# Kernel tuning notes

Hardware: AMD Instinct MI355X
Metric: run time of the kernel (lower is better)

The kernel has to match this reference:

```python
import jax, jax.numpy as jnp
import numpy as np

N = 100000      # nodes
E = 1000000     # edges
IN = 128        # input features
H = 64          # hidden_channels
EPS = 1e-5      # BatchNorm eps


def _gcn_conv(x, W, b, src, dst, n):
    # PyG GCNConv: linear -> add self loops -> sym-norm -> scatter-add -> bias
    h = x @ W                                   # [n, H]
    loop = jnp.arange(n)
    s = jnp.concatenate([src, loop])            # [E+n]
    d = jnp.concatenate([dst, loop])
    deg = jax.ops.segment_sum(jnp.ones(s.shape, h.dtype), d, num_segments=n)
    dinv = jnp.where(deg > 0, jax.lax.rsqrt(deg), 0.0)
    norm = dinv[s] * dinv[d]                    # [E+n]
    out = jax.ops.segment_sum(h[s] * norm[:, None], d, num_segments=n)
    return out + b


def _bn_relu(x, gamma, beta):
    # BatchNorm1d, training-mode batch statistics (biased var), then ReLU
    m = x.mean(axis=0)
    v = x.var(axis=0)
    return jax.nn.relu((x - m) * jax.lax.rsqrt(v + EPS) * gamma + beta)


def setup_inputs() -> dict:
    key = jax.random.key(0)
    ks = jax.random.split(key, 10)
    x = jax.random.normal(ks[0], (N, IN), jnp.float32)
    edge_index = jax.random.randint(ks[1], (2, E), 0, N)
    W1 = jax.random.normal(ks[2], (IN, H), jnp.float32) / np.sqrt(IN)
    b1 = jnp.zeros((H,), jnp.float32)
    g1 = jnp.ones((H,), jnp.float32)
    bt1 = jnp.zeros((H,), jnp.float32)
    W2 = jax.random.normal(ks[3], (H, H), jnp.float32) / np.sqrt(H)
    b2 = jnp.zeros((H,), jnp.float32)
    g2 = jnp.ones((H,), jnp.float32)
    bt2 = jnp.zeros((H,), jnp.float32)
    return {"x": x, "edge_index": edge_index, "W1": W1, "b1": b1,
            "g1": g1, "bt1": bt1, "W2": W2, "b2": b2, "g2": g2, "bt2": bt2}


def reference(x, edge_index, W1, b1, g1, bt1, W2, b2, g2, bt2):
    src, dst = edge_index[0], edge_index[1]
    n = x.shape[0]
    h = _gcn_conv(x, W1, b1, src, dst, n)
    h = _bn_relu(h, g1, bt1)          # dropout omitted (deterministic reference)
    h = _gcn_conv(h, W2, b2, src, dst, n)
    h = _bn_relu(h, g2, bt2)
    return h
```

## Files before the change

kernel.cpp:

```cpp
#include <hip/hip_runtime.h>


#define IN_F 128
#define HID  64
#define SCAN_CHUNK 512
static constexpr float BN_EPS = 1e-5f;

typedef float f32x4 __attribute__((ext_vector_type(4)));
typedef short bf16x8 __attribute__((ext_vector_type(8)));

__device__ inline unsigned short f2bf(float f) {
    union { float f; unsigned u; } v; v.f = f;
    unsigned r = v.u + 0x7FFFu + ((v.u >> 16) & 1u);
    return (unsigned short)(r >> 16);
}
__device__ inline float bf2f(unsigned short h) {
    union { unsigned u; float f; } v; v.u = (unsigned)h << 16;
    return v.f;
}
__device__ inline float bflo(unsigned v) {
    union { unsigned u; float f; } x; x.u = v << 16; return x.f;
}
__device__ inline float bfhi(unsigned v) {
    union { unsigned u; float f; } x; x.u = v & 0xffff0000u; return x.f;
}


__global__ void count_dst(const int* __restrict__ dst, int* __restrict__ counts, int E) {
    int e = blockIdx.x * blockDim.x + threadIdx.x;
    if (e < E) atomicAdd(&counts[dst[e]], 1);
}

__global__ void scan_block_reduce(const int* __restrict__ counts, int* __restrict__ blockSums, int n) {
    __shared__ int red[256];
    int base = blockIdx.x * SCAN_CHUNK;
    int t = threadIdx.x;
    int i0 = base + 2 * t, i1 = i0 + 1;
    int v = 0;
    if (i0 < n) v += counts[i0];
    if (i1 < n) v += counts[i1];
    red[t] = v;
    __syncthreads();
    for (int st = 128; st > 0; st >>= 1) {
        if (t < st) red[t] += red[t + st];
        __syncthreads();
    }
    if (t == 0) blockSums[blockIdx.x] = red[0];
}

__global__ void scan_top(const int* __restrict__ blockSums, int* __restrict__ blockOffs, int B) {
    __shared__ int a[2][256];
    int t = threadIdx.x;
    int v = (t < B) ? blockSums[t] : 0;
    int pin = 0;
    a[0][t] = v;
    __syncthreads();
    for (int st = 1; st < 256; st <<= 1) {
        int x = a[pin][t];
        if (t >= st) x += a[pin][t - st];
        a[pin ^ 1][t] = x;
        pin ^= 1;
        __syncthreads();
    }
    if (t < B) blockOffs[t] = a[pin][t] - v;
}

__global__ void scan_write(const int* __restrict__ counts, const int* __restrict__ blockOffs,
                           int* __restrict__ ptr, int* __restrict__ cursor,
                           float* __restrict__ dinv, int n) {
    __shared__ int a[2][256];
    int base = blockIdx.x * SCAN_CHUNK;
    int t = threadIdx.x;
    int i0 = base + 2 * t, i1 = i0 + 1;
    int c0 = (i0 < n) ? counts[i0] : 0;
    int c1 = (i1 < n) ? counts[i1] : 0;
    int s = c0 + c1;
    int pin = 0;
    a[0][t] = s;
    __syncthreads();
    for (int st = 1; st < 256; st <<= 1) {
        int x = a[pin][t];
        if (t >= st) x += a[pin][t - st];
        a[pin ^ 1][t] = x;
        pin ^= 1;
        __syncthreads();
    }
    int excl = a[pin][t] - s + blockOffs[blockIdx.x];
    if (i0 < n) {
        ptr[i0] = excl; cursor[i0] = excl;
        dinv[i0] = rsqrtf((float)c0 + 1.0f);
    }
    if (i1 < n) {
        ptr[i1] = excl + c0; cursor[i1] = excl + c0;
        dinv[i1] = rsqrtf((float)c1 + 1.0f);
    }
}

__global__ void fill_csr(const int* __restrict__ src, const int* __restrict__ dst,
                         int* __restrict__ cursor, int* __restrict__ csr, int E) {
    int e = blockIdx.x * blockDim.x + threadIdx.x;
    if (e < E) {
        int pos = atomicAdd(&cursor[dst[e]], 1);
        csr[pos] = src[e];
    }
}


__global__ void convert_w(const float* __restrict__ W1, const float* __restrict__ W2,
                          unsigned short* __restrict__ W1t, unsigned short* __restrict__ W2t) {
    int t = threadIdx.x;
    for (int i = t; i < HID * IN_F; i += 256) {
        int c = i >> 7, k = i & 127;
        W1t[i] = f2bf(W1[k * HID + c]);
    }
    for (int i = t; i < HID * HID; i += 256) {
        int c = i >> 6, k = i & 63;
        W2t[i] = f2bf(W2[k * HID + c]);
    }
}


template <int K>
__global__ __launch_bounds__(256) void mfma_gemm_x(
    const float* __restrict__ X, const unsigned short* __restrict__ Wt,
    const float* __restrict__ dinv, unsigned short* __restrict__ out, int n) {
    constexpr int KS = K / 32;
    int t = threadIdx.x;
    int lane = t & 63, l15 = lane & 15, lhi = lane >> 4;
    bf16x8 Bf[4][KS];
#pragma unroll
    for (int cb = 0; cb < 4; ++cb)
#pragma unroll
        for (int ks = 0; ks < KS; ++ks)
            Bf[cb][ks] = *(const bf16x8*)&Wt[(cb * 16 + l15) * K + ks * 32 + lhi * 8];

    int wid = blockIdx.x * 4 + (t >> 6);
    int ntiles = n >> 4;
    if (wid >= ntiles) return;
    int r0 = wid << 4;
    const float* xrow = X + (size_t)(r0 + l15) * K;
    bf16x8 Af[KS];
#pragma unroll
    for (int ks = 0; ks < KS; ++ks) {
        float4 u = *(const float4*)&xrow[ks * 32 + lhi * 8];
        float4 v = *(const float4*)&xrow[ks * 32 + lhi * 8 + 4];
        bf16x8 a;
        a[0] = f2bf(u.x); a[1] = f2bf(u.y); a[2] = f2bf(u.z); a[3] = f2bf(u.w);
        a[4] = f2bf(v.x); a[5] = f2bf(v.y); a[6] = f2bf(v.z); a[7] = f2bf(v.w);
        Af[ks] = a;
    }
    f32x4 acc[4] = {{0.f,0.f,0.f,0.f},{0.f,0.f,0.f,0.f},{0.f,0.f,0.f,0.f},{0.f,0.f,0.f,0.f}};
#pragma unroll
    for (int cb = 0; cb < 4; ++cb)
#pragma unroll
        for (int ks = 0; ks < KS; ++ks)
            acc[cb] = __builtin_amdgcn_mfma_f32_16x16x32_bf16(Af[ks], Bf[cb][ks], acc[cb], 0, 0, 0);
#pragma unroll
    for (int j = 0; j < 4; ++j) {
        int r = r0 + lhi * 4 + j;
        float dv = dinv[r];
#pragma unroll
        for (int cb = 0; cb < 4; ++cb)
            out[(size_t)r * HID + cb * 16 + l15] = f2bf(acc[cb][j] * dv);
    }
}

__global__ __launch_bounds__(256) void mfma_gemm_bn(
    const float* __restrict__ V, const float* __restrict__ stats,
    const float* __restrict__ g, const float* __restrict__ beta,
    const unsigned short* __restrict__ Wt, const float* __restrict__ dinv,
    unsigned short* __restrict__ out, int n) {
    int t = threadIdx.x;
    int lane = t & 63, l15 = lane & 15, lhi = lane >> 4;
    bf16x8 Bf[4][2];
#pragma unroll
    for (int cb = 0; cb < 4; ++cb)
#pragma unroll
        for (int ks = 0; ks < 2; ++ks)
            Bf[cb][ks] = *(const bf16x8*)&Wt[(cb * 16 + l15) * HID + ks * 32 + lhi * 8];

    float aK[2][8], bK[2][8];
    float inv_n = 1.0f / (float)n;
#pragma unroll
    for (int ks = 0; ks < 2; ++ks)
#pragma unroll
        for (int e = 0; e < 8; ++e) {
            int k = ks * 32 + lhi * 8 + e;
            float m = stats[k] * inv_n;
            float var = stats[HID + k] * inv_n - m * m;
            float a = g[k] * rsqrtf(var + BN_EPS);
            aK[ks][e] = a;
            bK[ks][e] = beta[k] - m * a;
        }

    int wid = blockIdx.x * 4 + (t >> 6);
    int ntiles = n >> 4;
    if (wid >= ntiles) return;
    int r0 = wid << 4;
    const float* vrow = V + (size_t)(r0 + l15) * HID;
    bf16x8 Af[2];
#pragma unroll
    for (int ks = 0; ks < 2; ++ks) {
        float4 u = *(const float4*)&vrow[ks * 32 + lhi * 8];
        float4 v = *(const float4*)&vrow[ks * 32 + lhi * 8 + 4];
        float y[8] = {u.x, u.y, u.z, u.w, v.x, v.y, v.z, v.w};
        bf16x8 a;
#pragma unroll
        for (int e = 0; e < 8; ++e)
            a[e] = f2bf(fmaxf(fmaf(y[e], aK[ks][e], bK[ks][e]), 0.0f));
        Af[ks] = a;
    }
    f32x4 acc[4] = {{0.f,0.f,0.f,0.f},{0.f,0.f,0.f,0.f},{0.f,0.f,0.f,0.f},{0.f,0.f,0.f,0.f}};
#pragma unroll
    for (int cb = 0; cb < 4; ++cb)
#pragma unroll
        for (int ks = 0; ks < 2; ++ks)
            acc[cb] = __builtin_amdgcn_mfma_f32_16x16x32_bf16(Af[ks], Bf[cb][ks], acc[cb], 0, 0, 0);
#pragma unroll
    for (int j = 0; j < 4; ++j) {
        int r = r0 + lhi * 4 + j;
        float dv = dinv[r];
#pragma unroll
        for (int cb = 0; cb < 4; ++cb)
            out[(size_t)r * HID + cb * 16 + l15] = f2bf(acc[cb][j] * dv);
    }
}


__global__ __launch_bounds__(256) void aggregate_stats_bf(
    const unsigned short* __restrict__ hs, const float* __restrict__ dinv,
    const int* __restrict__ ptr, const int* __restrict__ counts,
    const int* __restrict__ csr, float* __restrict__ agg,
    float* __restrict__ stats, int n) {
    int t = threadIdx.x;
    int lane32 = t & 31;
    int grp = (blockIdx.x * blockDim.x + t) >> 5;
    int ngrp = (gridDim.x * blockDim.x) >> 5;
    float sx = 0.f, sy = 0.f, s2x = 0.f, s2y = 0.f;
    for (int i = grp; i < n; i += ngrp) {
        unsigned v = *(const unsigned*)&hs[(size_t)i * HID + 2 * lane32];
        float ax = bflo(v), ay = bfhi(v);
        float bx = 0.f, by = 0.f, cx = 0.f, cy = 0.f, dx = 0.f, dy = 0.f;
        int b = ptr[i], cnt = counts[i];
        int k = 0;
        while (k < cnt) {
            int take = min(cnt - k, 32);
            int idx = (lane32 < take) ? csr[b + k + lane32] : 0;
            int j = 0;
            for (; j + 4 <= take; j += 4) {
                int s0 = __shfl(idx, j + 0, 32);
                int s1 = __shfl(idx, j + 1, 32);
                int s2 = __shfl(idx, j + 2, 32);
                int s3 = __shfl(idx, j + 3, 32);
                unsigned v0 = *(const unsigned*)&hs[(size_t)s0 * HID + 2 * lane32];
                unsigned v1 = *(const unsigned*)&hs[(size_t)s1 * HID + 2 * lane32];
                unsigned v2 = *(const unsigned*)&hs[(size_t)s2 * HID + 2 * lane32];
                unsigned v3 = *(const unsigned*)&hs[(size_t)s3 * HID + 2 * lane32];
                ax += bflo(v0); ay += bfhi(v0);
                bx += bflo(v1); by += bfhi(v1);
                cx += bflo(v2); cy += bfhi(v2);
                dx += bflo(v3); dy += bfhi(v3);
            }
            for (; j < take; ++j) {
                int s0 = __shfl(idx, j, 32);
                unsigned v0 = *(const unsigned*)&hs[(size_t)s0 * HID + 2 * lane32];
                ax += bflo(v0); ay += bfhi(v0);
            }
            k += take;
        }
        float di = dinv[i];
        float ox = (ax + bx + cx + dx) * di;
        float oy = (ay + by + cy + dy) * di;
        *(float2*)&agg[(size_t)i * HID + 2 * lane32] = make_float2(ox, oy);
        sx += ox; sy += oy;
        s2x += ox * ox; s2y += oy * oy;
    }
    __shared__ float ls[8][HID];
    __shared__ float ls2[8][HID];
    int hg = t >> 5;
    ls[hg][2 * lane32]      = sx;  ls[hg][2 * lane32 + 1]  = sy;
    ls2[hg][2 * lane32]     = s2x; ls2[hg][2 * lane32 + 1] = s2y;
    __syncthreads();
    if (t < HID) {
        float ts = 0.f, t2 = 0.f;
#pragma unroll
        for (int q = 0; q < 8; ++q) { ts += ls[q][t]; t2 += ls2[q][t]; }
        atomicAdd(&stats[t], ts);
        atomicAdd(&stats[HID + t], t2);
    }
}

__global__ void bn_apply_relu4(const float* __restrict__ v, const float* __restrict__ stats,
                               const float* __restrict__ g, const float* __restrict__ beta,
                               float* __restrict__ out, int n) {
    int i = blockIdx.x * blockDim.x + threadIdx.x;
    if (i >= n * (HID / 4)) return;
    int c4 = (i & 15) << 2;
    float inv_n = 1.0f / (float)n;
    float4 vv = ((const float4*)v)[i];
    float o[4];
    float xs[4] = {vv.x, vv.y, vv.z, vv.w};
#pragma unroll
    for (int j = 0; j < 4; ++j) {
        int c = c4 + j;
        float m = stats[c] * inv_n;
        float var = stats[HID + c] * inv_n - m * m;
        float a = g[c] * rsqrtf(var + BN_EPS);
        float y = (xs[j] - m) * a + beta[c];
        o[j] = y > 0.0f ? y : 0.0f;
    }
    ((float4*)out)[i] = make_float4(o[0], o[1], o[2], o[3]);
}


extern "C" void kernel_launch(void* const* d_in, const int* in_sizes, int n_in,
                              void* d_out, int out_size, void* d_ws, size_t ws_size,
                              hipStream_t stream) {
    const float* x   = (const float*)d_in[0];
    const int*   ei  = (const int*)d_in[1];
    const float* W1  = (const float*)d_in[2];
    const float* g1  = (const float*)d_in[4];
    const float* bt1 = (const float*)d_in[5];
    const float* W2  = (const float*)d_in[6];
    const float* g2  = (const float*)d_in[8];
    const float* bt2 = (const float*)d_in[9];

    const int n = in_sizes[0] / IN_F;
    const int E = in_sizes[1] / 2;
    const int* src = ei;
    const int* dst = ei + E;

    char* w = (char*)d_ws;
    int*            counts    = (int*)w;            w += (size_t)n * 4;
    int*            ptr       = (int*)w;            w += (size_t)n * 4;
    int*            cursor    = (int*)w;            w += (size_t)n * 4;
    float*          dinv      = (float*)w;          w += (size_t)n * 4;
    int*            blockSums = (int*)w;            w += 256 * 4;
    int*            blockOffs = (int*)w;            w += 256 * 4;
    float*          stats     = (float*)w;          w += 256 * 4;
    unsigned short* W1t       = (unsigned short*)w; w += (size_t)HID * IN_F * 2;
    unsigned short* W2t       = (unsigned short*)w; w += (size_t)HID * HID * 2;
    int*            csr       = (int*)w;            w += (size_t)E * 4;
    unsigned short* hs        = (unsigned short*)w; w += (size_t)n * HID * 2;
    float*          aggF      = (float*)w;

    hipMemsetAsync(counts, 0, (size_t)n * 4, stream);
    hipMemsetAsync(stats, 0, 256 * 4, stream);

    const int B = (n + SCAN_CHUNK - 1) / SCAN_CHUNK;

    count_dst<<<(E + 255) / 256, 256, 0, stream>>>(dst, counts, E);
    scan_block_reduce<<<B, 256, 0, stream>>>(counts, blockSums, n);
    scan_top<<<1, 256, 0, stream>>>(blockSums, blockOffs, B);
    scan_write<<<B, 256, 0, stream>>>(counts, blockOffs, ptr, cursor, dinv, n);
    fill_csr<<<(E + 255) / 256, 256, 0, stream>>>(src, dst, cursor, csr, E);
    convert_w<<<1, 256, 0, stream>>>(W1, W2, W1t, W2t);

    const int ntiles = n >> 4;
    const int gblk = (ntiles + 3) / 4;

    mfma_gemm_x<IN_F><<<gblk, 256, 0, stream>>>(x, W1t, dinv, hs, n);
    aggregate_stats_bf<<<2048, 256, 0, stream>>>(hs, dinv, ptr, counts, csr, aggF, stats, n);

    mfma_gemm_bn<<<gblk, 256, 0, stream>>>(aggF, stats, g1, bt1, W2t, dinv, hs, n);
    aggregate_stats_bf<<<2048, 256, 0, stream>>>(hs, dinv, ptr, counts, csr, aggF, stats + 128, n);
    bn_apply_relu4<<<(n * (HID / 4) + 255) / 256, 256, 0, stream>>>(
        aggF, stats + 128, g2, bt2, (float*)d_out, n);
}
```

Before: 402.7 us.

## Store aggregation output in bf16, use 16-lane node groups, fuse weight convert

The intermediate aggregation buffer changes from fp32 to bf16, so the aggregate, GEMM-BN and final BN kernels move half the bytes for it. The gather kernel now handles one node per 16-lane group, with each lane loading 8-byte ushort4 chunks instead of 4-byte pairs, and per-group statistics are reduced in shared memory. The weight conversion is folded into an extra block of the degree-count kernel, removing one launch. Rounding the intermediate activations to bf16 adds precision loss before BatchNorm.

```diff
diff --git a/kernel.cpp b/kernel.cpp
--- a/kernel.cpp
+++ b/kernel.cpp
@@ -18,15 +18,23 @@
     union { unsigned u; float f; } v; v.u = (unsigned)h << 16;
     return v.f;
 }
-__device__ inline float bflo(unsigned v) {
-    union { unsigned u; float f; } x; x.u = v << 16; return x.f;
-}
-__device__ inline float bfhi(unsigned v) {
-    union { unsigned u; float f; } x; x.u = v & 0xffff0000u; return x.f;
-}
-
-
-__global__ void count_dst(const int* __restrict__ dst, int* __restrict__ counts, int E) {
+
+
+__global__ void count_dst_convw(const int* __restrict__ dst, int* __restrict__ counts, int E,
+                                const float* __restrict__ W1, const float* __restrict__ W2,
+                                unsigned short* __restrict__ W1t, unsigned short* __restrict__ W2t) {
+    if (blockIdx.x == gridDim.x - 1) {
+        int t = threadIdx.x;
+        for (int i = t; i < HID * IN_F; i += 256) {
+            int c = i >> 7, k = i & 127;
+            W1t[i] = f2bf(W1[k * HID + c]);
+        }
+        for (int i = t; i < HID * HID; i += 256) {
+            int c = i >> 6, k = i & 63;
+            W2t[i] = f2bf(W2[k * HID + c]);
+        }
+        return;
+    }
     int e = blockIdx.x * blockDim.x + threadIdx.x;
     if (e < E) atomicAdd(&counts[dst[e]], 1);
 }
@@ -106,20 +114,6 @@
 }
 
 
-__global__ void convert_w(const float* __restrict__ W1, const float* __restrict__ W2,
-                          unsigned short* __restrict__ W1t, unsigned short* __restrict__ W2t) {
-    int t = threadIdx.x;
-    for (int i = t; i < HID * IN_F; i += 256) {
-        int c = i >> 7, k = i & 127;
-        W1t[i] = f2bf(W1[k * HID + c]);
-    }
-    for (int i = t; i < HID * HID; i += 256) {
-        int c = i >> 6, k = i & 63;
-        W2t[i] = f2bf(W2[k * HID + c]);
-    }
-}
-
-
 template <int K>
 __global__ __launch_bounds__(256) void mfma_gemm_x(
     const float* __restrict__ X, const unsigned short* __restrict__ Wt,
@@ -166,7 +160,7 @@
 }
 
 __global__ __launch_bounds__(256) void mfma_gemm_bn(
-    const float* __restrict__ V, const float* __restrict__ stats,
+    const unsigned short* __restrict__ V, const float* __restrict__ stats,
     const float* __restrict__ g, const float* __restrict__ beta,
     const unsigned short* __restrict__ Wt, const float* __restrict__ dinv,
     unsigned short* __restrict__ out, int n) {
@@ -197,17 +191,17 @@
     int ntiles = n >> 4;
     if (wid >= ntiles) return;
     int r0 = wid << 4;
-    const float* vrow = V + (size_t)(r0 + l15) * HID;
+    const unsigned short* vrow = V + (size_t)(r0 + l15) * HID;
     bf16x8 Af[2];
 #pragma unroll
     for (int ks = 0; ks < 2; ++ks) {
-        float4 u = *(const float4*)&vrow[ks * 32 + lhi * 8];
-        float4 v = *(const float4*)&vrow[ks * 32 + lhi * 8 + 4];
-        float y[8] = {u.x, u.y, u.z, u.w, v.x, v.y, v.z, v.w};
+        bf16x8 raw = *(const bf16x8*)&vrow[ks * 32 + lhi * 8];
         bf16x8 a;
 #pragma unroll
-        for (int e = 0; e < 8; ++e)
-            a[e] = f2bf(fmaxf(fmaf(y[e], aK[ks][e], bK[ks][e]), 0.0f));
+        for (int e = 0; e < 8; ++e) {
+            float y = bf2f((unsigned short)raw[e]);
+            a[e] = f2bf(fmaxf(fmaf(y, aK[ks][e], bK[ks][e]), 0.0f));
+        }
         Af[ks] = a;
     }
     f32x4 acc[4] = {{0.f,0.f,0.f,0.f},{0.f,0.f,0.f,0.f},{0.f,0.f,0.f,0.f},{0.f,0.f,0.f,0.f}};
@@ -230,76 +224,85 @@
 __global__ __launch_bounds__(256) void aggregate_stats_bf(
     const unsigned short* __restrict__ hs, const float* __restrict__ dinv,
     const int* __restrict__ ptr, const int* __restrict__ counts,
-    const int* __restrict__ csr, float* __restrict__ agg,
+    const int* __restrict__ csr, unsigned short* __restrict__ agg,
     float* __restrict__ stats, int n) {
     int t = threadIdx.x;
-    int lane32 = t & 31;
-    int grp = (blockIdx.x * blockDim.x + t) >> 5;
-    int ngrp = (gridDim.x * blockDim.x) >> 5;
-    float sx = 0.f, sy = 0.f, s2x = 0.f, s2y = 0.f;
+    int l16 = t & 15;
+    int grp = (blockIdx.x * blockDim.x + t) >> 4;
+    int ngrp = (gridDim.x * blockDim.x) >> 4;
+    float st0 = 0.f, st1 = 0.f, st2 = 0.f, st3 = 0.f;
+    float sq0 = 0.f, sq1 = 0.f, sq2 = 0.f, sq3 = 0.f;
     for (int i = grp; i < n; i += ngrp) {
-        unsigned v = *(const unsigned*)&hs[(size_t)i * HID + 2 * lane32];
-        float ax = bflo(v), ay = bfhi(v);
-        float bx = 0.f, by = 0.f, cx = 0.f, cy = 0.f, dx = 0.f, dy = 0.f;
+        ushort4 sv = *(const ushort4*)&hs[(size_t)i * HID + 4 * l16];
+        float acc[4][4] = {};
+        acc[0][0] = bf2f(sv.x); acc[0][1] = bf2f(sv.y);
+        acc[0][2] = bf2f(sv.z); acc[0][3] = bf2f(sv.w);
         int b = ptr[i], cnt = counts[i];
         int k = 0;
         while (k < cnt) {
-            int take = min(cnt - k, 32);
-            int idx = (lane32 < take) ? csr[b + k + lane32] : 0;
+            int take = min(cnt - k, 16);
+            int idx = (l16 < take) ? csr[b + k + l16] : 0;
             int j = 0;
             for (; j + 4 <= take; j += 4) {
-                int s0 = __shfl(idx, j + 0, 32);
-                int s1 = __shfl(idx, j + 1, 32);
-                int s2 = __shfl(idx, j + 2, 32);
-                int s3 = __shfl(idx, j + 3, 32);
-                unsigned v0 = *(const unsigned*)&hs[(size_t)s0 * HID + 2 * lane32];
-                unsigned v1 = *(const unsigned*)&hs[(size_t)s1 * HID + 2 * lane32];
-                unsigned v2 = *(const unsigned*)&hs[(size_t)s2 * HID + 2 * lane32];
-                unsigned v3 = *(const unsigned*)&hs[(size_t)s3 * HID + 2 * lane32];
-                ax += bflo(v0); ay += bfhi(v0);
-                bx += bflo(v1); by += bfhi(v1);
-                cx += bflo(v2); cy += bfhi(v2);
-                dx += bflo(v3); dy += bfhi(v3);
+                ushort4 vv[4];
+#pragma unroll
+                for (int u = 0; u < 4; ++u) {
+                    int sI = __shfl(idx, j + u, 16);
+                    vv[u] = *(const ushort4*)&hs[(size_t)sI * HID + 4 * l16];
+                }
+#pragma unroll
+                for (int u = 0; u < 4; ++u) {
+                    acc[u][0] += bf2f(vv[u].x); acc[u][1] += bf2f(vv[u].y);
+                    acc[u][2] += bf2f(vv[u].z); acc[u][3] += bf2f(vv[u].w);
+                }
             }
             for (; j < take; ++j) {
-                int s0 = __shfl(idx, j, 32);
-                unsigned v0 = *(const unsigned*)&hs[(size_t)s0 * HID + 2 * lane32];
-                ax += bflo(v0); ay += bfhi(v0);
+                int sI = __shfl(idx, j, 16);
+                ushort4 vv = *(const ushort4*)&hs[(size_t)sI * HID + 4 * l16];
+                acc[0][0] += bf2f(vv.x); acc[0][1] += bf2f(vv.y);
+                acc[0][2] += bf2f(vv.z); acc[0][3] += bf2f(vv.w);
             }
             k += take;
         }
         float di = dinv[i];
-        float ox = (ax + bx + cx + dx) * di;
-        float oy = (ay + by + cy + dy) * di;
-        *(float2*)&agg[(size_t)i * HID + 2 * lane32] = make_float2(ox, oy);
-        sx += ox; sy += oy;
-        s2x += ox * ox; s2y += oy * oy;
-    }
-    __shared__ float ls[8][HID];
-    __shared__ float ls2[8][HID];
-    int hg = t >> 5;
-    ls[hg][2 * lane32]      = sx;  ls[hg][2 * lane32 + 1]  = sy;
-    ls2[hg][2 * lane32]     = s2x; ls2[hg][2 * lane32 + 1] = s2y;
+        float o0 = (acc[0][0] + acc[1][0] + acc[2][0] + acc[3][0]) * di;
+        float o1 = (acc[0][1] + acc[1][1] + acc[2][1] + acc[3][1]) * di;
+        float o2 = (acc[0][2] + acc[1][2] + acc[2][2] + acc[3][2]) * di;
+        float o3 = (acc[0][3] + acc[1][3] + acc[2][3] + acc[3][3]) * di;
+        ushort4 ov;
+        ov.x = f2bf(o0); ov.y = f2bf(o1); ov.z = f2bf(o2); ov.w = f2bf(o3);
+        *(ushort4*)&agg[(size_t)i * HID + 4 * l16] = ov;
+        st0 += o0; st1 += o1; st2 += o2; st3 += o3;
+        sq0 += o0 * o0; sq1 += o1 * o1; sq2 += o2 * o2; sq3 += o3 * o3;
+    }
+    __shared__ float ls[16][HID];
+    __shared__ float ls2[16][HID];
+    int gb = t >> 4;
+    ls[gb][4 * l16 + 0] = st0; ls[gb][4 * l16 + 1] = st1;
+    ls[gb][4 * l16 + 2] = st2; ls[gb][4 * l16 + 3] = st3;
+    ls2[gb][4 * l16 + 0] = sq0; ls2[gb][4 * l16 + 1] = sq1;
+    ls2[gb][4 * l16 + 2] = sq2; ls2[gb][4 * l16 + 3] = sq3;
     __syncthreads();
     if (t < HID) {
         float ts = 0.f, t2 = 0.f;
 #pragma unroll
-        for (int q = 0; q < 8; ++q) { ts += ls[q][t]; t2 += ls2[q][t]; }
+        for (int q = 0; q < 16; ++q) { ts += ls[q][t]; t2 += ls2[q][t]; }
         atomicAdd(&stats[t], ts);
         atomicAdd(&stats[HID + t], t2);
     }
 }
 
-__global__ void bn_apply_relu4(const float* __restrict__ v, const float* __restrict__ stats,
-                               const float* __restrict__ g, const float* __restrict__ beta,
-                               float* __restrict__ out, int n) {
+__global__ void bn_apply_relu_bf(const unsigned short* __restrict__ v,
+                                 const float* __restrict__ stats,
+                                 const float* __restrict__ g, const float* __restrict__ beta,
+                                 float* __restrict__ out, int n) {
     int i = blockIdx.x * blockDim.x + threadIdx.x;
     if (i >= n * (HID / 4)) return;
     int c4 = (i & 15) << 2;
     float inv_n = 1.0f / (float)n;
-    float4 vv = ((const float4*)v)[i];
+    ushort4 vv = ((const ushort4*)v)[i];
+    float xs[4] = {bf2f(vv.x), bf2f(vv.y), bf2f(vv.z), bf2f(vv.w)};
     float o[4];
-    float xs[4] = {vv.x, vv.y, vv.z, vv.w};
 #pragma unroll
     for (int j = 0; j < 4; ++j) {
         int c = c4 + j;
@@ -342,28 +345,27 @@
     unsigned short* W2t       = (unsigned short*)w; w += (size_t)HID * HID * 2;
     int*            csr       = (int*)w;            w += (size_t)E * 4;
     unsigned short* hs        = (unsigned short*)w; w += (size_t)n * HID * 2;
-    float*          aggF      = (float*)w;
+    unsigned short* aggB      = (unsigned short*)w;
 
     hipMemsetAsync(counts, 0, (size_t)n * 4, stream);
     hipMemsetAsync(stats, 0, 256 * 4, stream);
 
     const int B = (n + SCAN_CHUNK - 1) / SCAN_CHUNK;
 
-    count_dst<<<(E + 255) / 256, 256, 0, stream>>>(dst, counts, E);
+    count_dst_convw<<<(E + 255) / 256 + 1, 256, 0, stream>>>(dst, counts, E, W1, W2, W1t, W2t);
     scan_block_reduce<<<B, 256, 0, stream>>>(counts, blockSums, n);
     scan_top<<<1, 256, 0, stream>>>(blockSums, blockOffs, B);
     scan_write<<<B, 256, 0, stream>>>(counts, blockOffs, ptr, cursor, dinv, n);
     fill_csr<<<(E + 255) / 256, 256, 0, stream>>>(src, dst, cursor, csr, E);
-    convert_w<<<1, 256, 0, stream>>>(W1, W2, W1t, W2t);
 
     const int ntiles = n >> 4;
     const int gblk = (ntiles + 3) / 4;
 
     mfma_gemm_x<IN_F><<<gblk, 256, 0, stream>>>(x, W1t, dinv, hs, n);
-    aggregate_stats_bf<<<2048, 256, 0, stream>>>(hs, dinv, ptr, counts, csr, aggF, stats, n);
-
-    mfma_gemm_bn<<<gblk, 256, 0, stream>>>(aggF, stats, g1, bt1, W2t, dinv, hs, n);
-    aggregate_stats_bf<<<2048, 256, 0, stream>>>(hs, dinv, ptr, counts, csr, aggF, stats + 128, n);
-    bn_apply_relu4<<<(n * (HID / 4) + 255) / 256, 256, 0, stream>>>(
-        aggF, stats + 128, g2, bt2, (float*)d_out, n);
-}
+    aggregate_stats_bf<<<2048, 256, 0, stream>>>(hs, dinv, ptr, counts, csr, aggB, stats, n);
+
+    mfma_gemm_bn<<<gblk, 256, 0, stream>>>(aggB, stats, g1, bt1, W2t, dinv, hs, n);
+    aggregate_stats_bf<<<2048, 256, 0, stream>>>(hs, dinv, ptr, counts, csr, aggB, stats + 128, n);
+    bn_apply_relu_bf<<<(n * (HID / 4) + 255) / 256, 256, 0, stream>>>(
+        aggB, stats + 128, g2, bt2, (float*)d_out, n);
+}
```

Result: faster. 391.6 us (-2.8%).
